# Kernel tuning notes

Measured on AMD Instinct MI355X. Metric: run time of the kernel, lower is better.

The kernel has to match this reference:

```python
import jax, jax.numpy as jnp
import numpy as np

THETA = 10000.0

def _rope(x, pos):
    # x: [b, h, s, hd]; pos: [s]
    hd = x.shape[-1]
    inv_freq = 1.0 / (THETA ** (jnp.arange(0, hd, 2, dtype=jnp.float32) / hd))  # [hd/2]
    ang = pos.astype(jnp.float32)[:, None] * inv_freq[None, :]                   # [s, hd/2]
    cos, sin = jnp.cos(ang), jnp.sin(ang)
    x1, x2 = x[..., 0::2], x[..., 1::2]
    r1 = x1 * cos - x2 * sin
    r2 = x1 * sin + x2 * cos
    return jnp.stack([r1, r2], axis=-1).reshape(x.shape)

def setup_inputs() -> dict:
    key = jax.random.key(0)
    ks = jax.random.split(key, 5)
    b, s, d = 2, 2048, 1024
    scale = 0.02
    return {
        "x": jax.random.normal(ks[0], (b, s, d), dtype=jnp.float32),
        "Wq": jax.random.normal(ks[1], (d, d), dtype=jnp.float32) * scale,
        "Wk": jax.random.normal(ks[2], (d, d), dtype=jnp.float32) * scale,
        "Wv": jax.random.normal(ks[3], (d, d), dtype=jnp.float32) * scale,
        "Wo": jax.random.normal(ks[4], (d, d), dtype=jnp.float32) * scale,
    }

def reference(x, Wq, Wk, Wv, Wo):
    b, s, d = x.shape
    n_heads = 16
    hd = d // n_heads

    def split_heads(t):  # [b,s,d] -> [b,h,s,hd]
        return t.reshape(b, s, n_heads, hd).transpose(0, 2, 1, 3)

    q = split_heads(x @ Wq.T)
    k = split_heads(x @ Wk.T)
    v = split_heads(x @ Wv.T)

    pos = jnp.arange(s)
    q = _rope(q, pos)
    k = _rope(k, pos)

    scores = jnp.einsum("bhqd,bhkd->bhqk", q, k) / jnp.sqrt(jnp.float32(hd))
    causal = jnp.tril(jnp.ones((s, s), dtype=bool))
    scores = jnp.where(causal, scores, -jnp.inf)
    attn = jax.nn.softmax(scores, axis=-1)
    ctx = jnp.einsum("bhqk,bhkd->bhqd", attn, v)
    ctx = ctx.transpose(0, 2, 1, 3).reshape(b, s, d)
    return ctx @ Wo.T
```

## Files before the change

kernel.cpp:

```cpp
#include <hip/hip_runtime.h>
#include <math.h>

#define B  2
#define S  2048
#define D  1024
#define NH 16
#define HD 64
#define NROWS (B * S)

#define AS1 __attribute__((address_space(1)))
#define AS3 __attribute__((address_space(3)))
#define GLD16(g, l) __builtin_amdgcn_global_load_lds((const AS1 void*)(g), (AS3 void*)(l), 16, 0, 0)

typedef __attribute__((ext_vector_type(8))) short short8;
typedef __attribute__((ext_vector_type(4))) float floatx4;

#define MFMA16(a, b, c) __builtin_amdgcn_mfma_f32_16x16x32_bf16((a), (b), (c), 0, 0, 0)

__device__ inline float fexp2(float x) { return __builtin_amdgcn_exp2f(x); }

__device__ inline unsigned short f2bf(float f) {
    union { float f; unsigned int u; } v; v.f = f;
    unsigned int u = v.u;
    u += 0x7fffu + ((u >> 16) & 1);
    return (unsigned short)(u >> 16);
}

__device__ inline unsigned int pack2bf(float a, float b) {
    unsigned int ua = __float_as_uint(a) + 0x8000u;
    unsigned int ub = __float_as_uint(b) + 0x8000u;
    return __builtin_amdgcn_perm(ub, ua, 0x07060302u);
}

__global__ __launch_bounds__(256) void cvt_kernel(
    const float* __restrict__ x,  const float* __restrict__ Wq,
    const float* __restrict__ Wk, const float* __restrict__ Wv,
    const float* __restrict__ Wo,
    unsigned short* __restrict__ xb,  unsigned short* __restrict__ wqb,
    unsigned short* __restrict__ wkb, unsigned short* __restrict__ wvb,
    unsigned short* __restrict__ wob)
{
    size_t idx = (size_t)blockIdx.x * 256 + threadIdx.x;
    const float* src; unsigned short* dst; size_t off;
    if (idx < (1u << 20)) { src = x; dst = xb; off = idx << 2; }
    else {
        size_t r = idx - (1u << 20);
        int w = (int)(r >> 18);
        off = (r & ((1u << 18) - 1)) << 2;
        src = (w == 0) ? Wq : (w == 1) ? Wk : (w == 2) ? Wv : Wo;
        dst = (w == 0) ? wqb : (w == 1) ? wkb : (w == 2) ? wvb : wob;
    }
    float4 f = *(const float4*)(src + off);
    ushort4 o;
    o.x = f2bf(f.x); o.y = f2bf(f.y); o.z = f2bf(f.z); o.w = f2bf(f.w);
    *(ushort4*)(dst + off) = o;
}

#define GEMM_STAGE(Abase, Bbase, kk, AD, BD)                                   \
{                                                                              \
    GLD16(Abase + (size_t)row0 * D + (kk) + ko0, AD + seg0 * 512);             \
    GLD16(Abase + (size_t)row1 * D + (kk) + ko1, AD + (seg0 + 1) * 512);       \
    GLD16(Bbase + (size_t)row0 * D + (kk) + ko0, BD + seg0 * 512);             \
    GLD16(Bbase + (size_t)row1 * D + (kk) + ko1, BD + (seg0 + 1) * 512);       \
}

#define GEMM_COMPUTE(AC, BC)                                                   \
{                                                                              \
    short8 a[4], b[4];                                                         \
    _Pragma("unroll")                                                          \
    for (int mi = 0; mi < 4; ++mi)                                             \
        a[mi] = *(const short8*)&AC[(wm + mi * 16 + lm) * 32 + quad * 8];      \
    _Pragma("unroll")                                                          \
    for (int ni = 0; ni < 4; ++ni)                                             \
        b[ni] = *(const short8*)&BC[(wn + ni * 16 + lm) * 32 + quad * 8];      \
    _Pragma("unroll")                                                          \
    for (int mi = 0; mi < 4; ++mi)                                             \
        _Pragma("unroll")                                                      \
        for (int ni = 0; ni < 4; ++ni)                                         \
            acc[mi][ni] = MFMA16(b[ni], a[mi], acc[mi][ni]);      \
}

__global__ __launch_bounds__(256) void gemm_qkv_mfma(
    const unsigned short* __restrict__ xb,
    const unsigned short* __restrict__ wqb,
    const unsigned short* __restrict__ wkb,
    const unsigned short* __restrict__ wvb,
    unsigned short* __restrict__ Qo, unsigned short* __restrict__ Ko,
    unsigned short* __restrict__ Vo)
{
    __shared__ short As0[128 * 32];
    __shared__ short As1[128 * 32];
    __shared__ short Bs0[128 * 32];
    __shared__ short Bs1[128 * 32];

    const int t    = threadIdx.x;
    const int wave = t >> 6, lane = t & 63;
    const int i0   = blockIdx.x * 128;
    const int by   = blockIdx.y;
    const int mat  = by >> 3;
    const int j0   = (by & 7) * 128;
    const unsigned short* __restrict__ W = (mat == 0) ? wqb : (mat == 1) ? wkb : wvb;
    unsigned short* __restrict__ out = (mat == 0) ? Qo : (mat == 1) ? Ko : Vo;

    const int wm = (wave & 1) * 64, wn = (wave >> 1) * 64;
    const int lm = lane & 15, quad = lane >> 4;

    const int seg0 = wave * 2;
    const int c0   = seg0 * 64 + lane;
    const int row0 = c0 >> 2, ko0 = (c0 & 3) << 3;
    const int c1   = c0 + 64;
    const int row1 = c1 >> 2, ko1 = (c1 & 3) << 3;

    const unsigned short* Abase = xb + (size_t)i0 * D;
    const unsigned short* Bbase = W  + (size_t)j0 * D;

    floatx4 acc[4][4] = {};

    GEMM_STAGE(Abase, Bbase, 0, As0, Bs0);
    __syncthreads();
    for (int k0 = 0; k0 < D; k0 += 64) {
        GEMM_STAGE(Abase, Bbase, k0 + 32, As1, Bs1);
        GEMM_COMPUTE(As0, Bs0);
        __syncthreads();
        if (k0 + 64 < D) GEMM_STAGE(Abase, Bbase, k0 + 64, As0, Bs0);
        GEMM_COMPUTE(As1, Bs1);
        __syncthreads();
    }

    const int h = (j0 + wn) >> 6;
    if (mat < 2) {
        #pragma unroll
        for (int mi = 0; mi < 4; ++mi) {
            const int mg = i0 + wm + mi * 16 + lm;
            const int si = mg & (S - 1), bb = mg >> 11;
            unsigned short* orow = out + ((size_t)(bb * NH + h) * S + si) * HD;
            #pragma unroll
            for (int ni = 0; ni < 4; ++ni) {
                const int dim0 = ni * 16 + quad * 4;
                floatx4 v = acc[mi][ni];
                float rv[4];
                #pragma unroll
                for (int p = 0; p < 2; ++p) {
                    float invf = fexp2(-(float)(dim0 + 2 * p) *
                                       (13.287712379549449f / 64.0f));
                    float sn, cs;
                    __sincosf((float)si * invf, &sn, &cs);
                    float x1 = v[2 * p], x2 = v[2 * p + 1];
                    float r1 = x1 * cs - x2 * sn;
                    float r2 = x1 * sn + x2 * cs;
                    if (mat == 0) {
                        r1 *= 0.1803368801111204f;
                        r2 *= 0.1803368801111204f;
                    }
                    rv[2 * p] = r1; rv[2 * p + 1] = r2;
                }
                ushort4 pk;
                pk.x = f2bf(rv[0]); pk.y = f2bf(rv[1]);
                pk.z = f2bf(rv[2]); pk.w = f2bf(rv[3]);
                *(ushort4*)(orow + dim0) = pk;
            }
        }
    } else {
        #pragma unroll
        for (int mi = 0; mi < 4; ++mi) {
            const int mg = i0 + wm + mi * 16 + lm;
            const int si = mg & (S - 1), bb = mg >> 11;
            unsigned short* vb = out + (size_t)(bb * NH + h) * HD * S + si;
            #pragma unroll
            for (int ni = 0; ni < 4; ++ni) {
                #pragma unroll
                for (int p = 0; p < 4; ++p) {
                    const int d = ni * 16 + quad * 4 + p;
                    vb[(size_t)d * S] = f2bf(acc[mi][ni][p]);
                }
            }
        }
    }
}

__global__ __launch_bounds__(256) void gemm_out_mfma(
    const unsigned short* __restrict__ Cb,
    const unsigned short* __restrict__ wob,
    float* __restrict__ out)
{
    __shared__ short As0[128 * 32];
    __shared__ short As1[128 * 32];
    __shared__ short Bs0[128 * 32];
    __shared__ short Bs1[128 * 32];

    const int t    = threadIdx.x;
    const int wave = t >> 6, lane = t & 63;
    const int i0   = blockIdx.x * 128;
    const int j0   = blockIdx.y * 128;

    const int wm = (wave & 1) * 64, wn = (wave >> 1) * 64;
    const int lm = lane & 15, quad = lane >> 4;

    const int seg0 = wave * 2;
    const int c0   = seg0 * 64 + lane;
    const int row0 = c0 >> 2, ko0 = (c0 & 3) << 3;
    const int c1   = c0 + 64;
    const int row1 = c1 >> 2, ko1 = (c1 & 3) << 3;

    const unsigned short* Abase = Cb  + (size_t)i0 * D;
    const unsigned short* Bbase = wob + (size_t)j0 * D;

    floatx4 acc[4][4] = {};

    GEMM_STAGE(Abase, Bbase, 0, As0, Bs0);
    __syncthreads();
    for (int k0 = 0; k0 < D; k0 += 64) {
        GEMM_STAGE(Abase, Bbase, k0 + 32, As1, Bs1);
        GEMM_COMPUTE(As0, Bs0);
        __syncthreads();
        if (k0 + 64 < D) GEMM_STAGE(Abase, Bbase, k0 + 64, As0, Bs0);
        GEMM_COMPUTE(As1, Bs1);
        __syncthreads();
    }

    #pragma unroll
    for (int mi = 0; mi < 4; ++mi) {
        const int mg = i0 + wm + mi * 16 + lm;
        float* orow = out + (size_t)mg * D;
        #pragma unroll
        for (int ni = 0; ni < 4; ++ni) {
            const int ng = j0 + wn + ni * 16 + quad * 4;
            *(floatx4*)(orow + ng) = acc[mi][ni];
        }
    }
}

#define ATTN_STEP(KC, VC, KN, VN)                                              \
{                                                                              \
    _Pragma("unroll")                                                          \
    for (int i = 0; i < 2; ++i) {                                              \
        int c = t + i * 256;                                                   \
        int row = c >> 3;                                                      \
        int dkc = (c & 7) ^ (row & 7);                                         \
        GLD16(Kg + (size_t)(k0n + row) * HD + dkc * 8, &KN[0][0] + c * 8);     \
        GLD16(Vg + (size_t)row * S + k0n + dkc * 8,    &VN[0][0] + c * 8);     \
    }                                                                          \
    short8 kb0[4], kb1[4];                                                     \
    _Pragma("unroll")                                                          \
    for (int nt = 0; nt < 4; ++nt) {                                           \
        kb0[nt] = *(const short8*)&KC[nt * 16 + lm][(quad ^ sw) * 8];          \
        kb1[nt] = *(const short8*)&KC[nt * 16 + lm][((4 + quad) ^ sw) * 8];    \
    }                                                                          \
    floatx4 sc[4];                                                             \
    _Pragma("unroll")                                                          \
    for (int nt = 0; nt < 4; ++nt) {                                           \
        floatx4 s = {0.f, 0.f, 0.f, 0.f};                                      \
        s = MFMA16(kb0[nt], qa0, s);                \
        s = MFMA16(kb1[nt], qa1, s);                                           \
        sc[nt] = s;                                                            \
    }                                                                          \
    if (diag) {                                                                \
        _Pragma("unroll")                                                      \
        for (int nt = 0; nt < 4; ++nt)                                         \
            _Pragma("unroll")                                                  \
            for (int r = 0; r < 4; ++r) {                                      \
                float pe = fexp2(sc[nt][r]);                                   \
                if (nt * 16 + quad * 4 + r > 16 * wave + lm) pe = 0.0f;        \
                sc[nt][r] = pe;                                                \
                lsum += pe;                                                    \
            }                                                                  \
    } else {                                                                   \
        _Pragma("unroll")                                                      \
        for (int nt = 0; nt < 4; ++nt)                                         \
            _Pragma("unroll")                                                  \
            for (int r = 0; r < 4; ++r) {                                      \
                float pe = fexp2(sc[nt][r]);                                   \
                sc[nt][r] = pe;                                                \
                lsum += pe;                                                    \
            }                                                                  \
    }                                                                          \
    _Pragma("unroll")                                                          \
    for (int nt = 0; nt < 4; ++nt) {                                           \
        uint2 pk;                                                              \
        pk.x = pack2bf(sc[nt][0], sc[nt][1]);                                  \
        pk.y = pack2bf(sc[nt][2], sc[nt][3]);                                  \
        int cp = (nt * 4 + quad) ^ psw;                                        \
        *(uint2*)&Ps[16 * wave + lm][cp * 4] = pk;                             \
    }                                                                          \
    short8 pa0 = *(const short8*)&Ps[16 * wave + lm][((quad * 2) ^ psw) * 4];  \
    short8 pa1 = *(const short8*)&Ps[16 * wave + lm][((8 + quad * 2) ^ psw) * 4]; \
    _Pragma("unroll")                                                          \
    for (int nt = 0; nt < 4; ++nt) {                                           \
        short8 vb0 = *(const short8*)&VC[nt * 16 + lm][(quad ^ sw) * 8];       \
        short8 vb1 = *(const short8*)&VC[nt * 16 + lm][((4 + quad) ^ sw) * 8]; \
        o[nt] = MFMA16(pa0, vb0, o[nt]);                                       \
        o[nt] = MFMA16(pa1, vb1, o[nt]);                                       \
    }                                                                          \
    __syncthreads();                                                           \
}

__global__ __launch_bounds__(256, 4) void attn_mfma(
    const unsigned short* __restrict__ Qb,
    const unsigned short* __restrict__ Kb,
    const unsigned short* __restrict__ Vt,
    unsigned short* __restrict__ Cb)
{
    __shared__ unsigned short Ks0[64][64];
    __shared__ unsigned short Ks1[64][64];
    __shared__ unsigned short Vs0[64][64];
    __shared__ unsigned short Vs1[64][64];
    __shared__ unsigned short Ps[64][64];

    const int t    = threadIdx.x;
    const int lane = t & 63, wave = t >> 6;
    const int lm   = lane & 15, quad = lane >> 4;
    const int sw   = lm & 7;
    const int psw  = (lm & 7) << 1;

    const int b     = blockIdx.x;
    const int bh    = b & 31;
    const int f     = (b >> 5) & 7;
    const int round = b >> 8;
    int qt;
    if      (round == 0) qt = f;
    else if (round == 1) qt = 15 - f;
    else if (round == 2) qt = 16 + f;
    else                 qt = 31 - f;
    const int q0 = qt * 64;

    const unsigned short* Qg = Qb + (size_t)bh * S * HD;
    const unsigned short* Kg = Kb + (size_t)bh * S * HD;
    const unsigned short* Vg = Vt + (size_t)bh * HD * S;

    short8 qa0 = *(const short8*)(Qg + (size_t)(q0 + 16 * wave + lm) * HD + quad * 8);
    short8 qa1 = *(const short8*)(Qg + (size_t)(q0 + 16 * wave + lm) * HD + 32 + quad * 8);

    #pragma unroll
    for (int i = 0; i < 2; ++i) {
        int c = t + i * 256;
        int row = c >> 3;
        int dkc = (c & 7) ^ (row & 7);
        GLD16(Kg + (size_t)row * HD + dkc * 8, &Ks0[0][0] + c * 8);
        GLD16(Vg + (size_t)row * S + dkc * 8,  &Vs0[0][0] + c * 8);
    }

    float lsum = 0.0f;
    floatx4 o[4] = {};

    __syncthreads();

    for (int kt = 0; kt <= qt; ++kt) {
        const int k0n = (kt + 1) * 64;
        const bool diag = (kt == qt);
        if ((kt & 1) == 0) ATTN_STEP(Ks0, Vs0, Ks1, Vs1)
        else               ATTN_STEP(Ks1, Vs1, Ks0, Vs0)
    }

    lsum += __shfl_xor(lsum, 16);
    lsum += __shfl_xor(lsum, 32);
    const int h = bh & (NH - 1), bb = bh >> 4;
    #pragma unroll
    for (int r = 0; r < 4; ++r) {
        float lr  = __shfl(lsum, (wave << 6 | (quad * 4 + r)) & 63);
        float inv = 1.0f / lr;
        size_t row = (size_t)bb * S + q0 + 16 * wave + quad * 4 + r;
        #pragma unroll
        for (int nt = 0; nt < 4; ++nt)
            Cb[row * D + h * HD + nt * 16 + lm] = f2bf(o[nt][r] * inv);
    }
}

extern "C" void kernel_launch(void* const* d_in, const int* in_sizes, int n_in,
                              void* d_out, int out_size, void* d_ws, size_t ws_size,
                              hipStream_t stream) {
    (void)in_sizes; (void)n_in; (void)out_size; (void)ws_size;
    const float* x  = (const float*)d_in[0];
    const float* Wq = (const float*)d_in[1];
    const float* Wk = (const float*)d_in[2];
    const float* Wv = (const float*)d_in[3];
    const float* Wo = (const float*)d_in[4];
    float* out = (float*)d_out;

    char* w = (char*)d_ws;
    unsigned short* Qb  = (unsigned short*)(w);
    unsigned short* Kb  = (unsigned short*)(w + (((size_t)8)  << 20));
    unsigned short* Vtb = (unsigned short*)(w + (((size_t)16) << 20));
    unsigned short* Cb  = (unsigned short*)(w + (((size_t)24) << 20));
    unsigned short* xb  = (unsigned short*)(w + (((size_t)32) << 20));
    unsigned short* wqb = (unsigned short*)(w + (((size_t)40) << 20));
    unsigned short* wkb = (unsigned short*)(w + (((size_t)42) << 20));
    unsigned short* wvb = (unsigned short*)(w + (((size_t)44) << 20));
    unsigned short* wob = (unsigned short*)(w + (((size_t)46) << 20));

    cvt_kernel<<<8192, 256, 0, stream>>>(x, Wq, Wk, Wv, Wo,
                                         xb, wqb, wkb, wvb, wob);

    dim3 g1(NROWS / 128, 24);
    gemm_qkv_mfma<<<g1, 256, 0, stream>>>(xb, wqb, wkb, wvb, Qb, Kb, Vtb);

    attn_mfma<<<1024, 256, 0, stream>>>(Qb, Kb, Vtb, Cb);

    dim3 g3(NROWS / 128, D / 128);
    gemm_out_mfma<<<g3, 256, 0, stream>>>(Cb, wob, out);
}
```

Measured before the change: 178.6 us.

## Shrink GEMM M-tile to 64 rows and use precomputed RoPE cos/sin table

```diff
diff --git a/kernel.cpp b/kernel.cpp
--- a/kernel.cpp
+++ b/kernel.cpp
@@ -38,9 +38,22 @@
     const float* __restrict__ Wo,
     unsigned short* __restrict__ xb,  unsigned short* __restrict__ wqb,
     unsigned short* __restrict__ wkb, unsigned short* __restrict__ wvb,
-    unsigned short* __restrict__ wob)
+    unsigned short* __restrict__ wob, float2* __restrict__ tab)
 {
     size_t idx = (size_t)blockIdx.x * 256 + threadIdx.x;
+    if (idx >= (2u << 20)) {
+        int tt = (int)(idx - (2u << 20));
+        int j  = tt >> 9;
+        int s0 = (tt & 511) << 2;
+        float invf = fexp2(-(float)j * (13.287712379549449f / 32.0f));
+        #pragma unroll
+        for (int p = 0; p < 4; ++p) {
+            float sn, cs;
+            __sincosf((float)(s0 + p) * invf, &sn, &cs);
+            tab[j * 2048 + s0 + p] = make_float2(cs, sn);
+        }
+        return;
+    }
     const float* src; unsigned short* dst; size_t off;
     if (idx < (1u << 20)) { src = x; dst = xb; off = idx << 2; }
     else {
@@ -56,123 +69,120 @@
     *(ushort4*)(dst + off) = o;
 }
 
-#define GEMM_STAGE(Abase, Bbase, kk, AD, BD)                                   \
+#define GSTAGE(Abase, Bbase, kk, AD, BD)                                       \
 {                                                                              \
-    GLD16(Abase + (size_t)row0 * D + (kk) + ko0, AD + seg0 * 512);             \
-    GLD16(Abase + (size_t)row1 * D + (kk) + ko1, AD + (seg0 + 1) * 512);       \
-    GLD16(Bbase + (size_t)row0 * D + (kk) + ko0, BD + seg0 * 512);             \
-    GLD16(Bbase + (size_t)row1 * D + (kk) + ko1, BD + (seg0 + 1) * 512);       \
-}
-
-#define GEMM_COMPUTE(AC, BC)                                                   \
+    GLD16(Abase + (size_t)rowA  * D + (kk) + koA,  AD + cA  * 8);              \
+    GLD16(Bbase + (size_t)rowB0 * D + (kk) + koB0, BD + cB0 * 8);              \
+    GLD16(Bbase + (size_t)rowB1 * D + (kk) + koB1, BD + cB1 * 8);              \
+}
+
+#define GCOMP(AC, BC)                                                          \
 {                                                                              \
-    short8 a[4], b[4];                                                         \
+    short8 a[4], b[2];                                                         \
     _Pragma("unroll")                                                          \
     for (int mi = 0; mi < 4; ++mi)                                             \
-        a[mi] = *(const short8*)&AC[(wm + mi * 16 + lm) * 32 + quad * 8];      \
-    _Pragma("unroll")                                                          \
-    for (int ni = 0; ni < 4; ++ni)                                             \
-        b[ni] = *(const short8*)&BC[(wn + ni * 16 + lm) * 32 + quad * 8];      \
+        a[mi] = *(const short8*)&AC[(mi * 16 + lm) * 32 + quad * 8];           \
+    _Pragma("unroll")                                                          \
+    for (int ni = 0; ni < 2; ++ni)                                             \
+        b[ni] = *(const short8*)&BC[(wave * 32 + ni * 16 + lm) * 32 + quad * 8]; \
     _Pragma("unroll")                                                          \
     for (int mi = 0; mi < 4; ++mi)                                             \
         _Pragma("unroll")                                                      \
-        for (int ni = 0; ni < 4; ++ni)                                         \
+        for (int ni = 0; ni < 2; ++ni)                                         \
             acc[mi][ni] = MFMA16(b[ni], a[mi], acc[mi][ni]);      \
 }
 
-__global__ __launch_bounds__(256) void gemm_qkv_mfma(
+#define GEMM_PREAMBLE                                                          \
+    const int t    = threadIdx.x;                                              \
+    const int wave = t >> 6, lane = t & 63;                                    \
+    const int lm   = lane & 15, quad = lane >> 4;                              \
+    const int cA   = wave * 64 + lane;                                         \
+    const int rowA = cA >> 2,  koA  = (cA & 3) << 3;                           \
+    const int cB0  = wave * 128 + lane;                                        \
+    const int rowB0 = cB0 >> 2, koB0 = (cB0 & 3) << 3;                         \
+    const int cB1  = cB0 + 64;                                                 \
+    const int rowB1 = cB1 >> 2, koB1 = (cB1 & 3) << 3;
+
+#define GEMM_KLOOP(Abase, Bbase)                                               \
+    GSTAGE(Abase, Bbase, 0, As0, Bs0);                                         \
+    __syncthreads();                                                           \
+    for (int k0 = 0; k0 < D; k0 += 64) {                                       \
+        GSTAGE(Abase, Bbase, k0 + 32, As1, Bs1);                               \
+        GCOMP(As0, Bs0);                                                       \
+        __syncthreads();                                                       \
+        if (k0 + 64 < D) GSTAGE(Abase, Bbase, k0 + 64, As0, Bs0);              \
+        GCOMP(As1, Bs1);                                                       \
+        __syncthreads();                                                       \
+    }
+
+__global__ __launch_bounds__(256, 5) void gemm_qkv_mfma(
     const unsigned short* __restrict__ xb,
     const unsigned short* __restrict__ wqb,
     const unsigned short* __restrict__ wkb,
     const unsigned short* __restrict__ wvb,
+    const float2* __restrict__ tab,
     unsigned short* __restrict__ Qo, unsigned short* __restrict__ Ko,
     unsigned short* __restrict__ Vo)
 {
-    __shared__ short As0[128 * 32];
-    __shared__ short As1[128 * 32];
+    __shared__ short As0[64 * 32];
+    __shared__ short As1[64 * 32];
     __shared__ short Bs0[128 * 32];
     __shared__ short Bs1[128 * 32];
 
-    const int t    = threadIdx.x;
-    const int wave = t >> 6, lane = t & 63;
-    const int i0   = blockIdx.x * 128;
-    const int by   = blockIdx.y;
-    const int mat  = by >> 3;
-    const int j0   = (by & 7) * 128;
+    GEMM_PREAMBLE
+    const int i0  = blockIdx.x * 64;
+    const int by  = blockIdx.y;
+    const int mat = by >> 3;
+    const int j0  = (by & 7) * 128;
     const unsigned short* __restrict__ W = (mat == 0) ? wqb : (mat == 1) ? wkb : wvb;
     unsigned short* __restrict__ out = (mat == 0) ? Qo : (mat == 1) ? Ko : Vo;
 
-    const int wm = (wave & 1) * 64, wn = (wave >> 1) * 64;
-    const int lm = lane & 15, quad = lane >> 4;
-
-    const int seg0 = wave * 2;
-    const int c0   = seg0 * 64 + lane;
-    const int row0 = c0 >> 2, ko0 = (c0 & 3) << 3;
-    const int c1   = c0 + 64;
-    const int row1 = c1 >> 2, ko1 = (c1 & 3) << 3;
-
     const unsigned short* Abase = xb + (size_t)i0 * D;
     const unsigned short* Bbase = W  + (size_t)j0 * D;
 
-    floatx4 acc[4][4] = {};
-
-    GEMM_STAGE(Abase, Bbase, 0, As0, Bs0);
-    __syncthreads();
-    for (int k0 = 0; k0 < D; k0 += 64) {
-        GEMM_STAGE(Abase, Bbase, k0 + 32, As1, Bs1);
-        GEMM_COMPUTE(As0, Bs0);
-        __syncthreads();
-        if (k0 + 64 < D) GEMM_STAGE(Abase, Bbase, k0 + 64, As0, Bs0);
-        GEMM_COMPUTE(As1, Bs1);
-        __syncthreads();
-    }
-
-    const int h = (j0 + wn) >> 6;
+    floatx4 acc[4][2] = {};
+    GEMM_KLOOP(Abase, Bbase)
+
+    const int h = (j0 + wave * 32) >> 6;
     if (mat < 2) {
         #pragma unroll
         for (int mi = 0; mi < 4; ++mi) {
-            const int mg = i0 + wm + mi * 16 + lm;
+            const int mg = i0 + mi * 16 + lm;
             const int si = mg & (S - 1), bb = mg >> 11;
             unsigned short* orow = out + ((size_t)(bb * NH + h) * S + si) * HD;
             #pragma unroll
-            for (int ni = 0; ni < 4; ++ni) {
-                const int dim0 = ni * 16 + quad * 4;
+            for (int ni = 0; ni < 2; ++ni) {
+                const int dim0 = (wave * 32 + ni * 16 + quad * 4) & 63;
+                const int j = dim0 >> 1;
+                float2 t0 = tab[j * 2048 + si];
+                float2 t1 = tab[(j + 1) * 2048 + si];
                 floatx4 v = acc[mi][ni];
-                float rv[4];
-                #pragma unroll
-                for (int p = 0; p < 2; ++p) {
-                    float invf = fexp2(-(float)(dim0 + 2 * p) *
-                                       (13.287712379549449f / 64.0f));
-                    float sn, cs;
-                    __sincosf((float)si * invf, &sn, &cs);
-                    float x1 = v[2 * p], x2 = v[2 * p + 1];
-                    float r1 = x1 * cs - x2 * sn;
-                    float r2 = x1 * sn + x2 * cs;
-                    if (mat == 0) {
-                        r1 *= 0.1803368801111204f;
-                        r2 *= 0.1803368801111204f;
-                    }
-                    rv[2 * p] = r1; rv[2 * p + 1] = r2;
+                float r0 = v[0] * t0.x - v[1] * t0.y;
+                float r1 = v[0] * t0.y + v[1] * t0.x;
+                float r2 = v[2] * t1.x - v[3] * t1.y;
+                float r3 = v[2] * t1.y + v[3] * t1.x;
+                if (mat == 0) {
+                    r0 *= 0.1803368801111204f; r1 *= 0.1803368801111204f;
+                    r2 *= 0.1803368801111204f; r3 *= 0.1803368801111204f;
                 }
                 ushort4 pk;
-                pk.x = f2bf(rv[0]); pk.y = f2bf(rv[1]);
-                pk.z = f2bf(rv[2]); pk.w = f2bf(rv[3]);
+                pk.x = f2bf(r0); pk.y = f2bf(r1);
+                pk.z = f2bf(r2); pk.w = f2bf(r3);
                 *(ushort4*)(orow + dim0) = pk;
             }
         }
     } else {
         #pragma unroll
         for (int mi = 0; mi < 4; ++mi) {
-            const int mg = i0 + wm + mi * 16 + lm;
+            const int mg = i0 + mi * 16 + lm;
             const int si = mg & (S - 1), bb = mg >> 11;
             unsigned short* vb = out + (size_t)(bb * NH + h) * HD * S + si;
             #pragma unroll
-            for (int ni = 0; ni < 4; ++ni) {
+            for (int ni = 0; ni < 2; ++ni) {
+                const int d0 = (wave * 32 + ni * 16 + quad * 4) & 63;
                 #pragma unroll
-                for (int p = 0; p < 4; ++p) {
-                    const int d = ni * 16 + quad * 4 + p;
-                    vb[(size_t)d * S] = f2bf(acc[mi][ni][p]);
-                }
+                for (int p = 0; p < 4; ++p)
+                    vb[(size_t)(d0 + p) * S] = f2bf(acc[mi][ni][p]);
             }
         }
     }
@@ -183,48 +193,28 @@
     const unsigned short* __restrict__ wob,
     float* __restrict__ out)
 {
-    __shared__ short As0[128 * 32];
-    __shared__ short As1[128 * 32];
+    __shared__ short As0[64 * 32];
+    __shared__ short As1[64 * 32];
     __shared__ short Bs0[128 * 32];
     __shared__ short Bs1[128 * 32];
 
-    const int t    = threadIdx.x;
-    const int wave = t >> 6, lane = t & 63;
-    const int i0   = blockIdx.x * 128;
-    const int j0   = blockIdx.y * 128;
-
-    const int wm = (wave & 1) * 64, wn = (wave >> 1) * 64;
-    const int lm = lane & 15, quad = lane >> 4;
-
-    const int seg0 = wave * 2;
-    const int c0   = seg0 * 64 + lane;
-    const int row0 = c0 >> 2, ko0 = (c0 & 3) << 3;
-    const int c1   = c0 + 64;
-    const int row1 = c1 >> 2, ko1 = (c1 & 3) << 3;
+    GEMM_PREAMBLE
+    const int i0 = blockIdx.x * 64;
+    const int j0 = blockIdx.y * 128;
 
     const unsigned short* Abase = Cb  + (size_t)i0 * D;
     const unsigned short* Bbase = wob + (size_t)j0 * D;
 
-    floatx4 acc[4][4] = {};
-
-    GEMM_STAGE(Abase, Bbase, 0, As0, Bs0);
-    __syncthreads();
-    for (int k0 = 0; k0 < D; k0 += 64) {
-        GEMM_STAGE(Abase, Bbase, k0 + 32, As1, Bs1);
-        GEMM_COMPUTE(As0, Bs0);
-        __syncthreads();
-        if (k0 + 64 < D) GEMM_STAGE(Abase, Bbase, k0 + 64, As0, Bs0);
-        GEMM_COMPUTE(As1, Bs1);
-        __syncthreads();
-    }
+    floatx4 acc[4][2] = {};
+    GEMM_KLOOP(Abase, Bbase)
 
     #pragma unroll
     for (int mi = 0; mi < 4; ++mi) {
-        const int mg = i0 + wm + mi * 16 + lm;
+        const int mg = i0 + mi * 16 + lm;
         float* orow = out + (size_t)mg * D;
         #pragma unroll
-        for (int ni = 0; ni < 4; ++ni) {
-            const int ng = j0 + wn + ni * 16 + quad * 4;
+        for (int ni = 0; ni < 2; ++ni) {
+            const int ng = j0 + wave * 32 + ni * 16 + quad * 4;
             *(floatx4*)(orow + ng) = acc[mi][ni];
         }
     }
@@ -386,15 +376,16 @@
     unsigned short* wkb = (unsigned short*)(w + (((size_t)42) << 20));
     unsigned short* wvb = (unsigned short*)(w + (((size_t)44) << 20));
     unsigned short* wob = (unsigned short*)(w + (((size_t)46) << 20));
-
-    cvt_kernel<<<8192, 256, 0, stream>>>(x, Wq, Wk, Wv, Wo,
-                                         xb, wqb, wkb, wvb, wob);
-
-    dim3 g1(NROWS / 128, 24);
-    gemm_qkv_mfma<<<g1, 256, 0, stream>>>(xb, wqb, wkb, wvb, Qb, Kb, Vtb);
+    float2*         tab = (float2*)(w + (((size_t)48) << 20));
+
+    cvt_kernel<<<8256, 256, 0, stream>>>(x, Wq, Wk, Wv, Wo,
+                                         xb, wqb, wkb, wvb, wob, tab);
+
+    dim3 g1(NROWS / 64, 24);
+    gemm_qkv_mfma<<<g1, 256, 0, stream>>>(xb, wqb, wkb, wvb, tab, Qb, Kb, Vtb);
 
     attn_mfma<<<1024, 256, 0, stream>>>(Qb, Kb, Vtb, Cb);
 
-    dim3 g3(NROWS / 128, D / 128);
+    dim3 g3(NROWS / 64, D / 128);
     gemm_out_mfma<<<g3, 256, 0, stream>>>(Cb, wob, out);
 }
```

Measured after the change: 177.4 us. No clear change (-0.7%).
